# Optimization experiments

Hardware: AMD Instinct MI355X
Metric: run time of the kernel (lower is better)

The kernel has to match this reference:

```python
import jax, jax.numpy as jnp
import numpy as np


def _conv1x1(W, x):
    # W: [out, in], x: [B, in, D, H, W] -> [B, out, D, H, W]
    return jnp.einsum('oc,bcdhw->bodhw', W, x)


def _maxpool2(x):
    # 2x2x2 max pool, stride 2, over the last three (spatial) dims
    return jax.lax.reduce_window(x, -jnp.inf, jax.lax.max,
                                 (1, 1, 2, 2, 2), (1, 1, 2, 2, 2), 'VALID')


def setup_inputs() -> dict:
    key = jax.random.key(0)
    ks = jax.random.split(key, 5)
    B, C, D, H, W = 4, 256, 24, 24, 24
    Cq = C // 8
    x = jax.random.normal(ks[0], (B, C, D, H, W), dtype=jnp.float32)
    Wf = jax.random.normal(ks[1], (Cq, C), dtype=jnp.float32) * (C ** -0.5)
    Wg = jax.random.normal(ks[2], (Cq, C), dtype=jnp.float32) * (C ** -0.5)
    Wh = jax.random.normal(ks[3], (Cq, C), dtype=jnp.float32) * (C ** -0.5)
    Wv = jax.random.normal(ks[4], (C, Cq), dtype=jnp.float32) * (Cq ** -0.5)
    gamma = jnp.ones((), dtype=jnp.float32)
    return {"x": x, "Wf": Wf, "Wg": Wg, "Wh": Wh, "Wv": Wv, "gamma": gamma}


def reference(x, Wf, Wg, Wh, Wv, gamma):
    B, C, D, H, W = x.shape
    Cq = Wf.shape[0]
    N = D * H * W          # query length
    M = N // 8

    f = _conv1x1(Wf, x).reshape(B, Cq, N)                 # [B, Cq, N]
    g = _maxpool2(_conv1x1(Wg, x)).reshape(B, Cq, M)      # [B, Cq, M]
    h = _maxpool2(_conv1x1(Wh, x)).reshape(B, Cq, M)      # [B, Cq, M]

    scores = jnp.einsum('bcn,bcm->bnm', f, g)             # [B, N, M]
    beta = jax.nn.softmax(scores, axis=-1)
    o = jnp.einsum('bcm,bnm->bcn', h, beta)               # [B, Cq, N]
    o = _conv1x1(Wv, o.reshape(B, Cq, D, H, W))           # [B, C, D, H, W]
    return gamma * o + x
```

## Files before the change

kernel.cpp:

```cpp
#include <hip/hip_runtime.h>

#define B 4
#define C 256
#define CQ 32
#define NN 13824
#define MM 1728
#define MS 12

typedef __attribute__((ext_vector_type(8))) short short8;
typedef __attribute__((ext_vector_type(4))) float float4_;
typedef __attribute__((ext_vector_type(16))) float floatx16;

static __device__ inline unsigned rne_bf16(float x) {
  unsigned u = __float_as_uint(x);
  u += 0x7FFFu + ((u >> 16) & 1u);
  return u >> 16;
}

static __device__ inline unsigned cvtpk(float lo, float hi) {
  unsigned r;
  asm("v_cvt_pk_bf16_f32 %0, %1, %2" : "=v"(r) : "v"(lo), "v"(hi));
  return r;
}

#define LOG2E 1.4426950408889634f
#define EXPOFS 43.28085122666891f

__global__ __launch_bounds__(256) void wcvt_kernel(
    const float* __restrict__ Wf, const float* __restrict__ Wg,
    const float* __restrict__ Wh, const float* __restrict__ Wv,
    unsigned short* __restrict__ W16c, unsigned short* __restrict__ Whv,
    unsigned short* __restrict__ Wlv) {
  const int i = blockIdx.x * 256 + threadIdx.x;
  if (i < 24576) {
    const int kk = i & 7;
    const int rest = i >> 3;
    const int m = rest % 96;
    const int r = rest / 96;
    const int kq = r & 3;
    const int ch = r >> 2;
    const int k = ch * 32 + kq * 8 + kk;
    const float* Wr = (m < 32) ? (Wf + m * C) : (m < 64) ? (Wg + (m - 32) * C)
                                                         : (Wh + (m - 64) * C);
    W16c[i] = (unsigned short)rne_bf16(Wr[k]);
  } else {
    const int j = i - 24576;
    const float v = Wv[j];
    const unsigned h = rne_bf16(v);
    Whv[j] = (unsigned short)h;
    Wlv[j] = (unsigned short)rne_bf16(v - __uint_as_float(h << 16));
  }
}

#define LOADX(SET, CH)                                                        \
  do {                                                                        \
    const float* xp = xbase4 + (size_t)((CH)*32 + kg * 4) * NN;               \
    _Pragma("unroll") for (int j = 0; j < 4; ++j)                             \
        vx4[SET][j] = *reinterpret_cast<const float4*>(xp + (size_t)j * NN);  \
  } while (0)

#define PACKX(SET, BUF)                                                       \
  do {                                                                        \
    _Pragma("unroll") for (int i = 0; i < 4; ++i) {                           \
      *reinterpret_cast<uint2*>(&xls[BUF][kg >> 1][nq * 4 + i][(kg & 1) * 4]) = \
          make_uint2(cvtpk(vx4[SET][0][i], vx4[SET][1][i]),                   \
                     cvtpk(vx4[SET][2][i], vx4[SET][3][i]));                  \
    }                                                                         \
  } while (0)

#define LOADW(CH)                                                             \
  do {                                                                        \
    const uint4* src = reinterpret_cast<const uint4*>(W16c + (size_t)(CH)*3072); \
    wr0 = src[t];                                                             \
    if (t < 128) wr1 = src[256 + t];                                          \
  } while (0)

#define STOREW(BUF)                                                           \
  do {                                                                        \
    uint4* dst = reinterpret_cast<uint4*>(&wls[BUF][0][0][0]);                \
    dst[t] = wr0;                                                             \
    if (t < 128) dst[256 + t] = wr1;                                          \
  } while (0)

#define COMPUTE(BUF)                                                          \
  do {                                                                        \
    _Pragma("unroll") for (int ks = 0; ks < 2; ++ks) {                        \
      const int kq = ks * 2 + hi;                                             \
      const short8 bfr =                                                      \
          *reinterpret_cast<const short8*>(&xls[BUF][kq][w * 32 + col][0]);   \
      const short8 a0 = *reinterpret_cast<const short8*>(&wls[BUF][kq][col][0]);      \
      const short8 a1 = *reinterpret_cast<const short8*>(&wls[BUF][kq][32 + col][0]); \
      const short8 a2 = *reinterpret_cast<const short8*>(&wls[BUF][kq][64 + col][0]); \
      accf = __builtin_amdgcn_mfma_f32_32x32x16_bf16(a0, bfr, accf, 0, 0, 0); \
      accg = __builtin_amdgcn_mfma_f32_32x32x16_bf16(a1, bfr, accg, 0, 0, 0); \
      acch = __builtin_amdgcn_mfma_f32_32x32x16_bf16(a2, bfr, acch, 0, 0, 0); \
    }                                                                         \
  } while (0)

__global__ __launch_bounds__(256) void proj_mfma(
    const float* __restrict__ x, const unsigned short* __restrict__ W16c,
    unsigned short* __restrict__ f16, unsigned short* __restrict__ g16,
    unsigned short* __restrict__ h16) {
  __shared__ __align__(16) unsigned short xls[2][4][128][8];
  __shared__ __align__(16) unsigned short wls[2][4][96][8];
  const int blk = blockIdx.x;
  const int b = blk / 108;
  const int n0 = (blk - b * 108) * 128;
  const int t = threadIdx.x;
  const int w = t >> 6, lane = t & 63;
  const int col = lane & 31, hi = lane >> 5;
  const int nq = t & 31, kg = t >> 5;

  floatx16 accf = {0}, accg = {0}, acch = {0};
  const float* xbase4 = x + ((size_t)b * C) * NN + n0 + nq * 4;
  float4 vx4[3][4];
  uint4 wr0, wr1;

  LOADX(0, 0);
  LOADX(1, 1);
  LOADX(2, 2);
  LOADW(0);
  PACKX(0, 0);
  STOREW(0);
  __syncthreads();

#pragma unroll
  for (int ch = 0; ch < 8; ++ch) {
    const int buf = ch & 1;
    if (ch + 1 < 8) LOADW(ch + 1);
    if (ch + 3 < 8) LOADX((ch + 3) % 3, ch + 3);
    COMPUTE(buf);
    if (ch + 1 < 8) {
      PACKX((ch + 1) % 3, buf ^ 1);
      STOREW(buf ^ 1);
      __syncthreads();
    }
  }

  const int n = n0 + w * 32 + col;
  {
    unsigned short* fp = f16 + ((size_t)b * NN + n) * 32 + hi * 4;
#pragma unroll
    for (int rp = 0; rp < 8; ++rp) {
      const int m = (rp & 1) * 2 + 8 * (rp >> 1);
      *reinterpret_cast<unsigned*>(fp + m) = cvtpk(accf[rp * 2], accf[rp * 2 + 1]);
    }
  }
  unsigned short* gp = g16 + (size_t)b * CQ * NN + n;
  unsigned short* hp = h16 + (size_t)b * CQ * NN + n;
#pragma unroll
  for (int r = 0; r < 16; ++r) {
    const int c = (r & 3) + 8 * (r >> 2) + 4 * hi;
    gp[(size_t)c * NN] = (unsigned short)rne_bf16(accg[r]);
    hp[(size_t)c * NN] = (unsigned short)rne_bf16(acch[r]);
  }
}

__global__ __launch_bounds__(256) void pool_kernel(
    const unsigned short* __restrict__ g16, const unsigned short* __restrict__ h16,
    unsigned short* __restrict__ gt16, unsigned short* __restrict__ ht16) {
  int i = blockIdx.x * 256 + threadIdx.x;
  const int m = i % MM;
  const int rest = i / MM;
  const int c = rest & 31;
  const int b = rest >> 5;
  const int wq = m % MS;
  const int hq = (m / MS) % MS;
  const int dq = m / (MS * MS);
  const size_t base = ((size_t)b * CQ + c) * NN +
                      (2 * dq) * 576 + (2 * hq) * 24 + (2 * wq);
  auto mx2 = [](unsigned u) {
    return fmaxf(__uint_as_float(u << 16), __uint_as_float(u & 0xFFFF0000u));
  };
  const unsigned short* pg = g16 + base;
  const unsigned short* ph = h16 + base;
  float vg = fmaxf(fmaxf(mx2(*(const unsigned*)(pg)),
                         mx2(*(const unsigned*)(pg + 24))),
                   fmaxf(mx2(*(const unsigned*)(pg + 576)),
                         mx2(*(const unsigned*)(pg + 600))));
  float vh = fmaxf(fmaxf(mx2(*(const unsigned*)(ph)),
                         mx2(*(const unsigned*)(ph + 24))),
                   fmaxf(mx2(*(const unsigned*)(ph + 576)),
                         mx2(*(const unsigned*)(ph + 600))));
  gt16[((size_t)b * MM + m) * 32 + c] = (unsigned short)(__float_as_uint(vg) >> 16);
  ht16[((size_t)b * 32 + c) * MM + m] = (unsigned short)(__float_as_uint(vh) >> 16);
}

__global__ __launch_bounds__(256, 4) void attn_kernel(
    const unsigned short* __restrict__ f16, const unsigned short* __restrict__ gt,
    const unsigned short* __restrict__ ht, const float* __restrict__ x,
    const unsigned short* __restrict__ Whv, const unsigned short* __restrict__ Wlv,
    const float* __restrict__ gamma, float* __restrict__ out) {
  __shared__ __align__(16) unsigned short sm[16896];
  const int blk = blockIdx.x;
  const int b = blk / 216;
  const int n0 = (blk - b * 216) * 64;
  const int t = threadIdx.x;
  const int w = t >> 6, L = t & 63, Q = L >> 4, col = L & 15;

  unsigned short* fls = sm;
  unsigned short* g0 = sm + 2560;
  unsigned short* g1 = sm + 5120;
  unsigned short* h0 = sm + 7680;
  unsigned short* h1 = sm + 9984;
  unsigned short* Pls = sm + 12288 + w * 1152;

  {
    const unsigned short* fsrc = f16 + ((size_t)(b * NN + n0)) * 32;
    *reinterpret_cast<uint4*>(fls + (t >> 2) * 40 + (t & 3) * 8) =
        *reinterpret_cast<const uint4*>(fsrc + t * 8);
  }
  const unsigned short* gsrc = gt + (size_t)b * MM * 32;
  const unsigned short* hsrc = ht + (size_t)b * 32 * MM;
  const int gk = t >> 2, gseg = t & 3;
  const int hc = t >> 3, hseg = t & 7;
  *reinterpret_cast<uint4*>(g0 + gk * 40 + gseg * 8) =
      *reinterpret_cast<const uint4*>(gsrc + gk * 32 + gseg * 8);
  *reinterpret_cast<uint4*>(h0 + hc * 72 + hseg * 8) =
      *reinterpret_cast<const uint4*>(hsrc + (size_t)hc * MM + hseg * 8);
  __syncthreads();

  const short8 fB = *reinterpret_cast<const short8*>(fls + (w * 16 + col) * 40 + Q * 8);

  float4_ acc0 = {0.f, 0.f, 0.f, 0.f}, acc1 = {0.f, 0.f, 0.f, 0.f};
  float l0 = 0.f, l1 = 0.f;

  for (int ch = 0; ch < 27; ++ch) {
    unsigned short* gcur = (ch & 1) ? g1 : g0;
    unsigned short* hcur = (ch & 1) ? h1 : h0;
    uint4 gnx, hnx;
    if (ch < 26) {
      const int k0 = (ch + 1) * 64;
      gnx = *reinterpret_cast<const uint4*>(gsrc + (size_t)(k0 + gk) * 32 + gseg * 8);
      hnx = *reinterpret_cast<const uint4*>(hsrc + (size_t)hc * MM + k0 + hseg * 8);
    }
    float4_ sc[4];
    __builtin_amdgcn_s_setprio(1);
#pragma unroll
    for (int T = 0; T < 4; ++T) {
      const short8 gA =
          *reinterpret_cast<const short8*>(gcur + (T * 16 + col) * 40 + Q * 8);
      float4_ z = {0.f, 0.f, 0.f, 0.f};
      sc[T] = __builtin_amdgcn_mfma_f32_16x16x32_bf16(gA, fB, z, 0, 0, 0);
    }
    __builtin_amdgcn_s_setprio(0);
#pragma unroll
    for (int T = 0; T < 4; ++T) {
      const float p0 = exp2f(fmaf(sc[T][0], LOG2E, -EXPOFS));
      const float p1 = exp2f(fmaf(sc[T][1], LOG2E, -EXPOFS));
      const float p2 = exp2f(fmaf(sc[T][2], LOG2E, -EXPOFS));
      const float p3 = exp2f(fmaf(sc[T][3], LOG2E, -EXPOFS));
      l0 += p0 + p1;
      l1 += p2 + p3;
      unsigned short* pw = Pls + col * 72 + T * 16 + Q * 4;
      *reinterpret_cast<uint2*>(pw) =
          make_uint2(cvtpk(p0, p1), cvtpk(p2, p3));
    }
#pragma unroll
    for (int ks = 0; ks < 2; ++ks) {
      const short8 pA =
          *reinterpret_cast<const short8*>(Pls + col * 72 + ks * 32 + Q * 8);
      const short8 hB0 =
          *reinterpret_cast<const short8*>(hcur + col * 72 + ks * 32 + Q * 8);
      const short8 hB1 =
          *reinterpret_cast<const short8*>(hcur + (16 + col) * 72 + ks * 32 + Q * 8);
      __builtin_amdgcn_s_setprio(1);
      acc0 = __builtin_amdgcn_mfma_f32_16x16x32_bf16(pA, hB0, acc0, 0, 0, 0);
      acc1 = __builtin_amdgcn_mfma_f32_16x16x32_bf16(pA, hB1, acc1, 0, 0, 0);
      __builtin_amdgcn_s_setprio(0);
    }
    if (ch < 26) {
      unsigned short* gnb = (ch & 1) ? g0 : g1;
      unsigned short* hnb = (ch & 1) ? h0 : h1;
      *reinterpret_cast<uint4*>(gnb + gk * 40 + gseg * 8) = gnx;
      *reinterpret_cast<uint4*>(hnb + hc * 72 + hseg * 8) = hnx;
    }
    __syncthreads();
  }

  float l = l0 + l1;
  l += __shfl_xor(l, 16);
  l += __shfl_xor(l, 32);
  float* ols = reinterpret_cast<float*>(sm);
#pragma unroll
  for (int r = 0; r < 4; ++r) {
    const float linv = 1.f / __shfl(l, Q * 4 + r);
    const int nl = w * 16 + Q * 4 + r;
    ols[nl * 33 + col] = acc0[r] * linv;
    ols[nl * 33 + 16 + col] = acc1[r] * linv;
  }
  __syncthreads();

  const int colA = L & 31, hiA = L >> 5;
  const float gm = gamma[0];
  short8 Bf[2][2];
#pragma unroll
  for (int nt = 0; nt < 2; ++nt) {
#pragma unroll
    for (int ks = 0; ks < 2; ++ks) {
      const float* p = &ols[(nt * 32 + colA) * 33 + ks * 16 + hiA * 8];
      uint4 uu;
      uu.x = cvtpk(p[0], p[1]);
      uu.y = cvtpk(p[2], p[3]);
      uu.z = cvtpk(p[4], p[5]);
      uu.w = cvtpk(p[6], p[7]);
      Bf[nt][ks] = *reinterpret_cast<short8*>(&uu);
    }
  }
#pragma unroll
  for (int tt = 0; tt < 2; ++tt) {
    const int ct = w + tt * 4;
    const int ca = ct * 32 + colA;
    const short8 Ah0 = *reinterpret_cast<const short8*>(Whv + ca * 32 + hiA * 8);
    const short8 Ah1 = *reinterpret_cast<const short8*>(Whv + ca * 32 + 16 + hiA * 8);
    const short8 Al0 = *reinterpret_cast<const short8*>(Wlv + ca * 32 + hiA * 8);
    const short8 Al1 = *reinterpret_cast<const short8*>(Wlv + ca * 32 + 16 + hiA * 8);
    floatx16 ac0 = {0}, ac1 = {0};
    __builtin_amdgcn_s_setprio(1);
    ac0 = __builtin_amdgcn_mfma_f32_32x32x16_bf16(Ah0, Bf[0][0], ac0, 0, 0, 0);
    ac0 = __builtin_amdgcn_mfma_f32_32x32x16_bf16(Ah1, Bf[0][1], ac0, 0, 0, 0);
    ac0 = __builtin_amdgcn_mfma_f32_32x32x16_bf16(Al0, Bf[0][0], ac0, 0, 0, 0);
    ac0 = __builtin_amdgcn_mfma_f32_32x32x16_bf16(Al1, Bf[0][1], ac0, 0, 0, 0);
    ac1 = __builtin_amdgcn_mfma_f32_32x32x16_bf16(Ah0, Bf[1][0], ac1, 0, 0, 0);
    ac1 = __builtin_amdgcn_mfma_f32_32x32x16_bf16(Ah1, Bf[1][1], ac1, 0, 0, 0);
    ac1 = __builtin_amdgcn_mfma_f32_32x32x16_bf16(Al0, Bf[1][0], ac1, 0, 0, 0);
    ac1 = __builtin_amdgcn_mfma_f32_32x32x16_bf16(Al1, Bf[1][1], ac1, 0, 0, 0);
    __builtin_amdgcn_s_setprio(0);
#pragma unroll
    for (int nt = 0; nt < 2; ++nt) {
      const floatx16 av = nt ? ac1 : ac0;
      const int n = n0 + nt * 32 + colA;
      const float* xp = x + ((size_t)b * C + ct * 32 + 4 * hiA) * NN + n;
      float* op = out + ((size_t)b * C + ct * 32 + 4 * hiA) * NN + n;
      float xv[16];
#pragma unroll
      for (int r = 0; r < 16; ++r)
        xv[r] = xp[(size_t)((r & 3) + 8 * (r >> 2)) * NN];
#pragma unroll
      for (int r = 0; r < 16; ++r)
        op[(size_t)((r & 3) + 8 * (r >> 2)) * NN] = gm * av[r] + xv[r];
    }
  }
}

extern "C" void kernel_launch(void* const* d_in, const int* in_sizes, int n_in,
                              void* d_out, int out_size, void* d_ws, size_t ws_size,
                              hipStream_t stream) {
  const float* x     = (const float*)d_in[0];
  const float* Wf    = (const float*)d_in[1];
  const float* Wg    = (const float*)d_in[2];
  const float* Wh    = (const float*)d_in[3];
  const float* Wv    = (const float*)d_in[4];
  const float* gamma = (const float*)d_in[5];
  float* out = (float*)d_out;
  float* ws = (float*)d_ws;

  unsigned short* f16  = (unsigned short*)ws;
  unsigned short* g16  = (unsigned short*)(ws + 884736);
  unsigned short* h16  = (unsigned short*)(ws + 1769472);
  unsigned short* Whv  = (unsigned short*)(ws + 2654208);
  unsigned short* Wlv  = (unsigned short*)(ws + 2658304);
  unsigned short* gt16 = (unsigned short*)(ws + 4423680);
  unsigned short* ht16 = (unsigned short*)(ws + 4534272);
  unsigned short* W16c = (unsigned short*)(ws + 4644864);

  wcvt_kernel<<<128, 256, 0, stream>>>(Wf, Wg, Wh, Wv, W16c, Whv, Wlv);
  proj_mfma<<<B * 108, 256, 0, stream>>>(x, W16c, f16, g16, h16);
  pool_kernel<<<(B * CQ * MM) / 256, 256, 0, stream>>>(g16, h16, gt16, ht16);
  attn_kernel<<<B * (NN / 64), 256, 0, stream>>>(f16, gt16, ht16, x, Whv, Wlv,
                                                 gamma, out);
}
```

Measured before the change: 159.4 us.

## Fuse weight bf16 conversion into projection and attention kernels, halve proj tile

Removes the separate weight-conversion kernel launch. The projection kernel now reads fp32 Wf/Wg/Wh directly and converts them to bf16 while staging into shared memory, and the attention epilogue splits Wv into hi/lo bf16 fragments on the fly. The projection kernel also moves to 128-thread blocks over 64 columns with twice as many blocks. This saves one launch and a small global round-trip, at the cost of redundant per-block fp32 weight loads and conversion ALU work.

```diff
diff --git a/kernel.cpp b/kernel.cpp
--- a/kernel.cpp
+++ b/kernel.cpp
@@ -26,32 +26,6 @@
 #define LOG2E 1.4426950408889634f
 #define EXPOFS 43.28085122666891f
 
-__global__ __launch_bounds__(256) void wcvt_kernel(
-    const float* __restrict__ Wf, const float* __restrict__ Wg,
-    const float* __restrict__ Wh, const float* __restrict__ Wv,
-    unsigned short* __restrict__ W16c, unsigned short* __restrict__ Whv,
-    unsigned short* __restrict__ Wlv) {
-  const int i = blockIdx.x * 256 + threadIdx.x;
-  if (i < 24576) {
-    const int kk = i & 7;
-    const int rest = i >> 3;
-    const int m = rest % 96;
-    const int r = rest / 96;
-    const int kq = r & 3;
-    const int ch = r >> 2;
-    const int k = ch * 32 + kq * 8 + kk;
-    const float* Wr = (m < 32) ? (Wf + m * C) : (m < 64) ? (Wg + (m - 32) * C)
-                                                         : (Wh + (m - 64) * C);
-    W16c[i] = (unsigned short)rne_bf16(Wr[k]);
-  } else {
-    const int j = i - 24576;
-    const float v = Wv[j];
-    const unsigned h = rne_bf16(v);
-    Whv[j] = (unsigned short)h;
-    Wlv[j] = (unsigned short)rne_bf16(v - __uint_as_float(h << 16));
-  }
-}
-
 #define LOADX(SET, CH)                                                        \
   do {                                                                        \
     const float* xp = xbase4 + (size_t)((CH)*32 + kg * 4) * NN;               \
@@ -70,16 +44,21 @@
 
 #define LOADW(CH)                                                             \
   do {                                                                        \
-    const uint4* src = reinterpret_cast<const uint4*>(W16c + (size_t)(CH)*3072); \
-    wr0 = src[t];                                                             \
-    if (t < 128) wr1 = src[256 + t];                                          \
+    _Pragma("unroll") for (int i = 0; i < 3; ++i) {                           \
+      wv[i][0] = *reinterpret_cast<const float4*>(wrow[i] + (CH)*32);         \
+      wv[i][1] = *reinterpret_cast<const float4*>(wrow[i] + (CH)*32 + 4);     \
+    }                                                                         \
   } while (0)
 
 #define STOREW(BUF)                                                           \
   do {                                                                        \
     uint4* dst = reinterpret_cast<uint4*>(&wls[BUF][0][0][0]);                \
-    dst[t] = wr0;                                                             \
-    if (t < 128) dst[256 + t] = wr1;                                          \
+    _Pragma("unroll") for (int i = 0; i < 3; ++i)                             \
+      dst[i * 128 + t] =                                                      \
+          make_uint4(cvtpk(wv[i][0].x, wv[i][0].y),                           \
+                     cvtpk(wv[i][0].z, wv[i][0].w),                           \
+                     cvtpk(wv[i][1].x, wv[i][1].y),                           \
+                     cvtpk(wv[i][1].z, wv[i][1].w));                          \
   } while (0)
 
 #define COMPUTE(BUF)                                                          \
@@ -97,24 +76,36 @@
     }                                                                         \
   } while (0)
 
-__global__ __launch_bounds__(256) void proj_mfma(
-    const float* __restrict__ x, const unsigned short* __restrict__ W16c,
+__global__ __launch_bounds__(128) void proj_mfma(
+    const float* __restrict__ x, const float* __restrict__ Wf,
+    const float* __restrict__ Wg, const float* __restrict__ Wh,
     unsigned short* __restrict__ f16, unsigned short* __restrict__ g16,
     unsigned short* __restrict__ h16) {
-  __shared__ __align__(16) unsigned short xls[2][4][128][8];
+  __shared__ __align__(16) unsigned short xls[2][4][64][8];
   __shared__ __align__(16) unsigned short wls[2][4][96][8];
   const int blk = blockIdx.x;
-  const int b = blk / 108;
-  const int n0 = (blk - b * 108) * 128;
+  const int b = blk / 216;
+  const int n0 = (blk - b * 216) * 64;
   const int t = threadIdx.x;
   const int w = t >> 6, lane = t & 63;
   const int col = lane & 31, hi = lane >> 5;
-  const int nq = t & 31, kg = t >> 5;
+  const int nq = t & 15, kg = t >> 4;
+
+  const float* wrow[3];
+#pragma unroll
+  for (int i = 0; i < 3; ++i) {
+    const int u = i * 128 + t;
+    const int kq = u / 96, m = u - kq * 96;
+    const float* base = (m < 32) ? (Wf + m * C)
+                      : (m < 64) ? (Wg + (m - 32) * C)
+                                 : (Wh + (m - 64) * C);
+    wrow[i] = base + kq * 8;
+  }
 
   floatx16 accf = {0}, accg = {0}, acch = {0};
   const float* xbase4 = x + ((size_t)b * C) * NN + n0 + nq * 4;
   float4 vx4[3][4];
-  uint4 wr0, wr1;
+  float4 wv[3][2];
 
   LOADX(0, 0);
   LOADX(1, 1);
@@ -186,11 +177,32 @@
   ht16[((size_t)b * 32 + c) * MM + m] = (unsigned short)(__float_as_uint(vh) >> 16);
 }
 
+static __device__ inline void dbl_frag(const float* __restrict__ p,
+                                       short8& hi8, short8& lo8) {
+  const float4 v0 = *reinterpret_cast<const float4*>(p);
+  const float4 v1 = *reinterpret_cast<const float4*>(p + 4);
+  uint4 h, l;
+  h.x = cvtpk(v0.x, v0.y);
+  h.y = cvtpk(v0.z, v0.w);
+  h.z = cvtpk(v1.x, v1.y);
+  h.w = cvtpk(v1.z, v1.w);
+  l.x = cvtpk(v0.x - __uint_as_float(h.x << 16),
+              v0.y - __uint_as_float(h.x & 0xFFFF0000u));
+  l.y = cvtpk(v0.z - __uint_as_float(h.y << 16),
+              v0.w - __uint_as_float(h.y & 0xFFFF0000u));
+  l.z = cvtpk(v1.x - __uint_as_float(h.z << 16),
+              v1.y - __uint_as_float(h.z & 0xFFFF0000u));
+  l.w = cvtpk(v1.z - __uint_as_float(h.w << 16),
+              v1.w - __uint_as_float(h.w & 0xFFFF0000u));
+  hi8 = *reinterpret_cast<short8*>(&h);
+  lo8 = *reinterpret_cast<short8*>(&l);
+}
+
 __global__ __launch_bounds__(256, 4) void attn_kernel(
     const unsigned short* __restrict__ f16, const unsigned short* __restrict__ gt,
     const unsigned short* __restrict__ ht, const float* __restrict__ x,
-    const unsigned short* __restrict__ Whv, const unsigned short* __restrict__ Wlv,
-    const float* __restrict__ gamma, float* __restrict__ out) {
+    const float* __restrict__ Wv, const float* __restrict__ gamma,
+    float* __restrict__ out) {
   __shared__ __align__(16) unsigned short sm[16896];
   const int blk = blockIdx.x;
   const int b = blk / 216;
@@ -311,10 +323,9 @@
   for (int tt = 0; tt < 2; ++tt) {
     const int ct = w + tt * 4;
     const int ca = ct * 32 + colA;
-    const short8 Ah0 = *reinterpret_cast<const short8*>(Whv + ca * 32 + hiA * 8);
-    const short8 Ah1 = *reinterpret_cast<const short8*>(Whv + ca * 32 + 16 + hiA * 8);
-    const short8 Al0 = *reinterpret_cast<const short8*>(Wlv + ca * 32 + hiA * 8);
-    const short8 Al1 = *reinterpret_cast<const short8*>(Wlv + ca * 32 + 16 + hiA * 8);
+    short8 Ah0, Al0, Ah1, Al1;
+    dbl_frag(Wv + ca * 32 + hiA * 8, Ah0, Al0);
+    dbl_frag(Wv + ca * 32 + 16 + hiA * 8, Ah1, Al1);
     floatx16 ac0 = {0}, ac1 = {0};
     __builtin_amdgcn_s_setprio(1);
     ac0 = __builtin_amdgcn_mfma_f32_32x32x16_bf16(Ah0, Bf[0][0], ac0, 0, 0, 0);
@@ -358,15 +369,11 @@
   unsigned short* f16  = (unsigned short*)ws;
   unsigned short* g16  = (unsigned short*)(ws + 884736);
   unsigned short* h16  = (unsigned short*)(ws + 1769472);
-  unsigned short* Whv  = (unsigned short*)(ws + 2654208);
-  unsigned short* Wlv  = (unsigned short*)(ws + 2658304);
   unsigned short* gt16 = (unsigned short*)(ws + 4423680);
   unsigned short* ht16 = (unsigned short*)(ws + 4534272);
-  unsigned short* W16c = (unsigned short*)(ws + 4644864);
-
-  wcvt_kernel<<<128, 256, 0, stream>>>(Wf, Wg, Wh, Wv, W16c, Whv, Wlv);
-  proj_mfma<<<B * 108, 256, 0, stream>>>(x, W16c, f16, g16, h16);
+
+  proj_mfma<<<B * 216, 128, 0, stream>>>(x, Wf, Wg, Wh, f16, g16, h16);
   pool_kernel<<<(B * CQ * MM) / 256, 256, 0, stream>>>(g16, h16, gt16, ht16);
-  attn_kernel<<<B * (NN / 64), 256, 0, stream>>>(f16, gt16, ht16, x, Whv, Wlv,
+  attn_kernel<<<B * (NN / 64), 256, 0, stream>>>(f16, gt16, ht16, x, Wv,
                                                  gamma, out);
 }
```

After: 169.3 us. 1.06x slower.
